# Performance work log

Measured on AMD Instinct MI355X. Metric: run time of the kernel, lower is better.

Reference implementation:

```python
import jax, jax.numpy as jnp
import numpy as np

D_MODEL = 4096
N_Q_HEAD = 32
N_KV_HEAD = 8
HEAD_DIM = D_MODEL // N_Q_HEAD  # 128
N_REP = N_Q_HEAD // N_KV_HEAD   # 4
B, T = 2, 2048


def _rope_tables(seq_len, head_dim, dtype=jnp.float32):
    # theta_i = 10000^(-2*(i-1)/d) for i=1..d/2  (matches torch.pow(10000, -2*(arange(1,d/2+1)-1)/d))
    i = jnp.arange(head_dim // 2, dtype=dtype)
    theta = jnp.power(10000.0, -2.0 * i / head_dim)
    angles = jnp.outer(jnp.arange(seq_len, dtype=dtype), theta)  # [T, d/2]
    return jnp.cos(angles), jnp.sin(angles)


def _apply_rope(x, cos, sin):
    # x: [B, T, h, HD]; pairs are consecutive elements (view_as_complex semantics)
    B_, T_, h, hd = x.shape
    xp = x.reshape(B_, T_, h, hd // 2, 2)
    xr, xi = xp[..., 0], xp[..., 1]
    c = cos[None, :T_, None, :]
    s = sin[None, :T_, None, :]
    out_r = xr * c - xi * s
    out_i = xr * s + xi * c
    return jnp.stack([out_r, out_i], axis=-1).reshape(B_, T_, h, hd)


def setup_inputs() -> dict:
    key = jax.random.key(0)
    ks = jax.random.split(key, 5)
    scale = 0.02
    x = jax.random.normal(ks[0], (B, T, D_MODEL), dtype=jnp.float32)
    wq = jax.random.normal(ks[1], (D_MODEL, N_Q_HEAD * HEAD_DIM), dtype=jnp.float32) * scale
    wk = jax.random.normal(ks[2], (D_MODEL, N_KV_HEAD * HEAD_DIM), dtype=jnp.float32) * scale
    wv = jax.random.normal(ks[3], (D_MODEL, N_KV_HEAD * HEAD_DIM), dtype=jnp.float32) * scale
    wo = jax.random.normal(ks[4], (N_Q_HEAD * HEAD_DIM, D_MODEL), dtype=jnp.float32) * scale
    # causal mask: 1 where masked (strict upper triangle), per masked_fill(mask==1, -inf)
    attention_mask = jnp.triu(jnp.ones((T, T), dtype=jnp.int32), k=1)
    return {"x": x, "wq": wq, "wk": wk, "wv": wv, "wo": wo, "attention_mask": attention_mask}


def reference(x, wq, wk, wv, wo, attention_mask):
    B_, T_, _ = x.shape
    xq = (x @ wq).reshape(B_, T_, N_Q_HEAD, HEAD_DIM)
    xk = (x @ wk).reshape(B_, T_, N_KV_HEAD, HEAD_DIM)
    xv = (x @ wv).reshape(B_, T_, N_KV_HEAD, HEAD_DIM)

    cos, sin = _rope_tables(T_, HEAD_DIM, x.dtype)
    xq = _apply_rope(xq, cos, sin)
    xk = _apply_rope(xk, cos, sin)

    # GQA: repeat kv heads (training path: no cache)
    xk = jnp.repeat(xk, N_REP, axis=2)  # [B, T, HQ, HD]
    xv = jnp.repeat(xv, N_REP, axis=2)

    q = xq.transpose(0, 2, 1, 3)  # [B, H, T, HD]
    k = xk.transpose(0, 2, 1, 3)
    v = xv.transpose(0, 2, 1, 3)

    scores = jnp.einsum('bhqd,bhkd->bhqk', q, k) / jnp.sqrt(jnp.asarray(HEAD_DIM, x.dtype))
    scores = jnp.where(attention_mask[None, None, :, :] == 1, -jnp.inf, scores)
    probs = jax.nn.softmax(scores, axis=-1)
    out = jnp.einsum('bhqk,bhkd->bhqd', probs, v)
    out = out.transpose(0, 2, 1, 3).reshape(B_, T_, N_Q_HEAD * HEAD_DIM)
    return out @ wo
```

## Files before the change

### kernel.cpp

```cpp
#include <hip/hip_runtime.h>
#include <hip/hip_bf16.h>
#include <math.h>

typedef __hip_bfloat16 bf16;
typedef short bf16x8 __attribute__((ext_vector_type(8)));
typedef float f32x4 __attribute__((ext_vector_type(4)));
typedef unsigned int u32;
typedef unsigned short u16;

#define GLD16(g, l)                                                            \
  __builtin_amdgcn_global_load_lds(                                            \
      (const __attribute__((address_space(1))) void*)(g),                      \
      (__attribute__((address_space(3))) void*)(l), 16, 0, 0)

__global__ void convert_f32_bf16(const float* __restrict__ in,
                                 bf16* __restrict__ out) {
  size_t i = ((size_t)blockIdx.x * 256 + threadIdx.x) * 4;
  float4 v = *(const float4*)(in + i);
  out[i + 0] = __float2bfloat16(v.x);
  out[i + 1] = __float2bfloat16(v.y);
  out[i + 2] = __float2bfloat16(v.z);
  out[i + 3] = __float2bfloat16(v.w);
}

__global__ void transpose_f32_bf16(const float* __restrict__ in,
                                   bf16* __restrict__ out, int R, int C) {
  __shared__ bf16 tile[32][33];
  int tx = threadIdx.x & 31, ty = threadIdx.x >> 5;
  int c0 = blockIdx.x * 32, r0 = blockIdx.y * 32;
#pragma unroll
  for (int i = 0; i < 32; i += 8)
    tile[ty + i][tx] = __float2bfloat16(in[(size_t)(r0 + ty + i) * C + c0 + tx]);
  __syncthreads();
#pragma unroll
  for (int i = 0; i < 32; i += 8)
    out[(size_t)(c0 + ty + i) * R + r0 + tx] = tile[tx][ty + i];
}

__global__ void transpose_v(const bf16* __restrict__ V, bf16* __restrict__ VT) {
  __shared__ bf16 tile[32][33];
  int s = blockIdx.z, b = s >> 3, kvh = s & 7;
  int t0 = blockIdx.x * 32, d0 = blockIdx.y * 32;
  int tx = threadIdx.x & 31, ty = threadIdx.x >> 5;
#pragma unroll
  for (int i = 0; i < 32; i += 8)
    tile[ty + i][tx] =
        V[(size_t)(b * 2048 + t0 + ty + i) * 6144 + kvh * 128 + d0 + tx];
  __syncthreads();
#pragma unroll
  for (int i = 0; i < 32; i += 8)
    VT[((size_t)s * 128 + d0 + ty + i) * 2048 + t0 + tx] = tile[tx][ty + i];
}

__global__ void rope_table_k(float* __restrict__ tab) {
  int idx = blockIdx.x * 256 + threadIdx.x;
  int t = idx >> 6, i = idx & 63;
  float theta = powf(10000.0f, -2.0f * (float)i / 128.0f);
  float ang = (float)t * theta;
  tab[idx * 2 + 0] = cosf(ang);
  tab[idx * 2 + 1] = sinf(ang);
}

__global__ void rope_apply(bf16* __restrict__ X, const float* __restrict__ tab,
                           int nheads, int rowstride, float omul) {
  size_t idx = (size_t)blockIdx.x * 256 + threadIdx.x;
  int i = (int)(idx & 63);
  size_t rest = idx >> 6;
  int h = (int)(rest % nheads);
  size_t r = rest / nheads;
  int t = (int)(r & 2047);
  float c = tab[(t * 64 + i) * 2 + 0];
  float s = tab[(t * 64 + i) * 2 + 1];
  bf16* p = X + r * (size_t)rowstride + h * 128 + 2 * i;
  float xr = __bfloat162float(p[0]), xi = __bfloat162float(p[1]);
  p[0] = __float2bfloat16((xr * c - xi * s) * omul);
  p[1] = __float2bfloat16((xr * s + xi * c) * omul);
}

template <typename OutT>
__global__ __launch_bounds__(256, 3) void gemm_bt(const bf16* __restrict__ A,
                                                  const bf16* __restrict__ BT,
                                                  OutT* __restrict__ C, int M,
                                                  int N, int K) {
  __shared__ bf16 As[128 * 32];
  __shared__ bf16 Bs[128 * 32];
  const int tid = threadIdx.x;
  const int lane = tid & 63, w = tid >> 6;
  const int wr = w >> 1, wc = w & 1;
  const int lr = lane & 15;
  const int ko = (lane >> 4) * 8;
  const int m0 = blockIdx.y * 128, n0 = blockIdx.x * 128;

  f32x4 acc[4][4];
#pragma unroll
  for (int m = 0; m < 4; ++m)
#pragma unroll
    for (int n = 0; n < 4; ++n)
#pragma unroll
      for (int j = 0; j < 4; ++j) acc[m][n][j] = 0.f;

  for (int k0 = 0; k0 < K; k0 += 32) {
#pragma unroll
    for (int i = 0; i < 2; ++i) {
      int c = i * 256 + tid;
      const bf16* ga = A + (size_t)(m0 + (c >> 2)) * K + k0 + (c & 3) * 8;
      const bf16* gb = BT + (size_t)(n0 + (c >> 2)) * K + k0 + (c & 3) * 8;
      GLD16(ga, As + c * 8);
      GLD16(gb, Bs + c * 8);
    }
    __syncthreads();
    bf16x8 af[4], bfr[4];
#pragma unroll
    for (int m = 0; m < 4; ++m)
      af[m] = *(const bf16x8*)(As + (wr * 64 + m * 16 + lr) * 32 + ko);
#pragma unroll
    for (int n = 0; n < 4; ++n)
      bfr[n] = *(const bf16x8*)(Bs + (wc * 64 + n * 16 + lr) * 32 + ko);
#pragma unroll
    for (int m = 0; m < 4; ++m)
#pragma unroll
      for (int n = 0; n < 4; ++n)
        acc[m][n] = __builtin_amdgcn_mfma_f32_16x16x32_bf16(af[m], bfr[n],
                                                            acc[m][n], 0, 0, 0);
    __syncthreads();
  }
#pragma unroll
  for (int m = 0; m < 4; ++m) {
    int row_base = m0 + wr * 64 + m * 16 + (lane >> 4) * 4;
#pragma unroll
    for (int n = 0; n < 4; ++n) {
      int col = n0 + wc * 64 + n * 16 + lr;
#pragma unroll
      for (int j = 0; j < 4; ++j) {
        float v = acc[m][n][j];
        if constexpr (sizeof(OutT) == 2)
          C[(size_t)(row_base + j) * N + col] = (OutT)__float2bfloat16(v);
        else
          C[(size_t)(row_base + j) * N + col] = (OutT)v;
      }
    }
  }
}

static __device__ inline u32 cvtpk_bf16(float a, float b) {
  u32 r;
  asm("v_cvt_pk_bf16_f32 %0, %1, %2" : "=v"(r) : "v"(a), "v"(b));
  return r;
}

__global__ __launch_bounds__(256) void flash_attn2(const bf16* __restrict__ Q,
                                                   const bf16* __restrict__ K,
                                                   const bf16* __restrict__ VT,
                                                   bf16* __restrict__ AO) {
  __shared__ bf16 Kbuf[2][64 * 128];
  __shared__ bf16 Vbuf[2][128 * 64];

  int bid = blockIdx.x;
  int lid = (bid & 7) * 128 + (bid >> 3);
  int qt = 15 - (lid & 15);
  int hq = (lid >> 4) & 3;
  int kvh = (lid >> 6) & 7;
  int b = lid >> 9;
  int h = kvh * 4 + hq;

  const int tid = threadIdx.x;
  const int lane = tid & 63, w = tid >> 6;
  const int lr = lane & 15, hi = lane >> 4;
  const int ko = hi * 8;
  const int qrow0 = qt * 128 + w * 32;
  const int nt = 2 * qt + 2;

  const bf16* Kg0 = K + (size_t)b * 2048 * 6144 + kvh * 128;
  const bf16* Vg0 = VT + (size_t)(b * 8 + kvh) * 128 * 2048;

  bf16x8 qf[2][4];
#pragma unroll
  for (int mi = 0; mi < 2; ++mi) {
    const bf16* qb = Q + (size_t)(b * 2048 + qrow0 + mi * 16 + lr) * 6144 + h * 128;
#pragma unroll
    for (int kk = 0; kk < 4; ++kk) qf[mi][kk] = *(const bf16x8*)(qb + kk * 32 + ko);
  }

  f32x4 O[2][8];
  float m_[2], l_[2];
#pragma unroll
  for (int mi = 0; mi < 2; ++mi) {
    m_[mi] = -1e30f;
    l_[mi] = 0.f;
#pragma unroll
    for (int dd = 0; dd < 8; ++dd)
#pragma unroll
      for (int j = 0; j < 4; ++j) O[mi][dd][j] = 0.f;
  }

  auto STAGE = [&](int buf, int kv0) {
    bf16* Ks = &Kbuf[buf][0];
    bf16* Vs = &Vbuf[buf][0];
    const bf16* Kg = Kg0 + (size_t)kv0 * 6144;
    const bf16* Vg = Vg0 + kv0;
#pragma unroll
    for (int it = 0; it < 4; ++it) {
      int s = it * 256 + tid;
      int row = s >> 4, c = s & 15;
      GLD16(Kg + (size_t)row * 6144 + ((c ^ (row & 7)) << 3), Ks + s * 8);
    }
#pragma unroll
    for (int it = 0; it < 4; ++it) {
      int s = it * 256 + tid;
      int row = s >> 3, c = s & 7;
      GLD16(Vg + (size_t)row * 2048 + ((c ^ (row & 7)) << 3), Vs + s * 8);
    }
  };

  STAGE(0, 0);
  __syncthreads();

  for (int t = 0; t < nt; ++t) {
    int kv0 = t * 64;
    if (t + 1 < nt) STAGE((t + 1) & 1, kv0 + 64);

    if (kv0 <= qrow0 + 31) {
      const bf16* Ks = &Kbuf[t & 1][0];
      const bf16* Vs = &Vbuf[t & 1][0];

      f32x4 Sx[2][4];
#pragma unroll
      for (int mi = 0; mi < 2; ++mi)
#pragma unroll
        for (int cb = 0; cb < 4; ++cb)
#pragma unroll
          for (int j = 0; j < 4; ++j) Sx[mi][cb][j] = 0.f;

      __builtin_amdgcn_s_setprio(1);
#pragma unroll
      for (int cb = 0; cb < 4; ++cb) {
        bf16x8 kf[4];
#pragma unroll
        for (int kk = 0; kk < 4; ++kk)
          kf[kk] = *(const bf16x8*)(Ks + (cb * 16 + lr) * 128 +
                                    (((kk * 4 + hi) ^ (lr & 7)) << 3));
#pragma unroll
        for (int mi = 0; mi < 2; ++mi)
#pragma unroll
          for (int kk = 0; kk < 4; ++kk)
            Sx[mi][cb] = __builtin_amdgcn_mfma_f32_16x16x32_bf16(
                kf[kk], qf[mi][kk], Sx[mi][cb], 0, 0, 0);
      }
      __builtin_amdgcn_s_setprio(0);

      bool domask = (kv0 + 63 > qrow0);
      u32 pau[2][2][4];
#pragma unroll
      for (int mi = 0; mi < 2; ++mi) {
        int q = qrow0 + mi * 16 + lr;
        if (domask) {
#pragma unroll
          for (int cb = 0; cb < 4; ++cb)
#pragma unroll
            for (int j = 0; j < 4; ++j)
              if (kv0 + cb * 16 + hi * 4 + j > q) Sx[mi][cb][j] = -1e30f;
        }
        float pm = -1e30f;
#pragma unroll
        for (int cb = 0; cb < 4; ++cb)
#pragma unroll
          for (int j = 0; j < 4; ++j) pm = fmaxf(pm, Sx[mi][cb][j]);
        pm = fmaxf(pm, __shfl_xor(pm, 16));
        pm = fmaxf(pm, __shfl_xor(pm, 32));

        if (!__all(pm - m_[mi] <= 11.5416f)) {
          float nm = fmaxf(m_[mi], pm);
          float rs = exp2f(m_[mi] - nm);
          m_[mi] = nm;
          l_[mi] *= rs;
#pragma unroll
          for (int dd = 0; dd < 8; ++dd)
#pragma unroll
            for (int j = 0; j < 4; ++j) O[mi][dd][j] *= rs;
        }
        float mcur = m_[mi];
        float ps = 0.f;
#pragma unroll
        for (int cb = 0; cb < 4; ++cb)
#pragma unroll
          for (int j = 0; j < 4; ++j) {
            float p = exp2f(Sx[mi][cb][j] - mcur);
            Sx[mi][cb][j] = p;
            ps += p;
          }
        ps += __shfl_xor(ps, 16);
        ps += __shfl_xor(ps, 32);
        l_[mi] += ps;

        u32 vp[8];
#pragma unroll
        for (int cb = 0; cb < 4; ++cb)
#pragma unroll
          for (int jp = 0; jp < 2; ++jp)
            vp[cb * 2 + jp] = cvtpk_bf16(Sx[mi][cb][2 * jp], Sx[mi][cb][2 * jp + 1]);

#pragma unroll
        for (int kk2 = 0; kk2 < 2; ++kk2)
#pragma unroll
          for (int e = 0; e < 4; ++e) {
            int src = lr + ((hi & 1) << 5) + ((e >> 1) << 4);
            u32 va = (u32)__shfl((int)vp[4 * kk2 + (e & 1)], src);
            u32 vb = (u32)__shfl((int)vp[4 * kk2 + 2 + (e & 1)], src);
            pau[mi][kk2][e] = (hi & 2) ? vb : va;
          }
      }

      __builtin_amdgcn_s_setprio(1);
#pragma unroll
      for (int dd = 0; dd < 8; ++dd) {
        bf16x8 vf[2];
#pragma unroll
        for (int kk2 = 0; kk2 < 2; ++kk2)
          vf[kk2] = *(const bf16x8*)(Vs + (dd * 16 + lr) * 64 +
                                     (((kk2 * 4 + hi) ^ (lr & 7)) << 3));
#pragma unroll
        for (int mi = 0; mi < 2; ++mi)
#pragma unroll
          for (int kk2 = 0; kk2 < 2; ++kk2) {
            union { u32 u[4]; bf16x8 h; } cv;
#pragma unroll
            for (int e = 0; e < 4; ++e) cv.u[e] = pau[mi][kk2][e];
            O[mi][dd] = __builtin_amdgcn_mfma_f32_16x16x32_bf16(
                vf[kk2], cv.h, O[mi][dd], 0, 0, 0);
          }
      }
      __builtin_amdgcn_s_setprio(0);
    }
    __syncthreads();
  }

#pragma unroll
  for (int mi = 0; mi < 2; ++mi) {
    float inv = 1.0f / l_[mi];
    bf16* outp = AO + (size_t)(b * 2048 + qrow0 + mi * 16 + lr) * 4096 + h * 128;
#pragma unroll
    for (int dd = 0; dd < 8; ++dd) {
      union { u16 s[4]; unsigned long long v; } pk;
#pragma unroll
      for (int j = 0; j < 4; ++j)
        pk.s[j] = __bfloat16_as_ushort(__float2bfloat16(O[mi][dd][j] * inv));
      *(unsigned long long*)(outp + dd * 16 + hi * 4) = pk.v;
    }
  }
}

extern "C" void kernel_launch(void* const* d_in, const int* in_sizes, int n_in,
                              void* d_out, int out_size, void* d_ws,
                              size_t ws_size, hipStream_t stream) {
  const float* x = (const float*)d_in[0];
  const float* wq = (const float*)d_in[1];
  const float* wk = (const float*)d_in[2];
  const float* wv = (const float*)d_in[3];
  const float* wo = (const float*)d_in[4];

  char* ws = (char*)d_ws;
  bf16* xb    = (bf16*)(ws + 0);
  bf16* WqkvT = (bf16*)(ws + 33554432);
  bf16* WoT   = (bf16*)(ws + 83886080);
  bf16* QKV   = (bf16*)(ws + 117440512);
  bf16* VTb   = (bf16*)(ws + 167772160);
  float* tab  = (float*)(ws + 176160768);
  bf16* AOb   = xb;

  const float LOG2E = 1.4426950408889634f;
  const float ISQ = 0.08838834764831845f;

  convert_f32_bf16<<<16384, 256, 0, stream>>>(x, xb);
  transpose_f32_bf16<<<dim3(128, 128), 256, 0, stream>>>(wq, WqkvT, 4096, 4096);
  transpose_f32_bf16<<<dim3(32, 128), 256, 0, stream>>>(
      wk, WqkvT + (size_t)4096 * 4096, 4096, 1024);
  transpose_f32_bf16<<<dim3(32, 128), 256, 0, stream>>>(
      wv, WqkvT + (size_t)5120 * 4096, 4096, 1024);
  transpose_f32_bf16<<<dim3(128, 128), 256, 0, stream>>>(wo, WoT, 4096, 4096);
  rope_table_k<<<512, 256, 0, stream>>>(tab);

  gemm_bt<bf16><<<dim3(48, 32), 256, 0, stream>>>(xb, WqkvT, QKV, 4096, 6144,
                                                  4096);

  rope_apply<<<32768, 256, 0, stream>>>(QKV, tab, 32, 6144, LOG2E * ISQ);
  rope_apply<<<8192, 256, 0, stream>>>(QKV + 4096, tab, 8, 6144, 1.0f);

  transpose_v<<<dim3(64, 4, 16), 256, 0, stream>>>(QKV + 5120, VTb);

  flash_attn2<<<1024, 256, 0, stream>>>(QKV, QKV + 4096, VTb, AOb);

  gemm_bt<float><<<dim3(32, 32), 256, 0, stream>>>(AOb, WoT, (float*)d_out,
                                                   4096, 4096, 4096);
}
```

Before: 718.2 us.

## Replace GEMM with 256x256 double-buffered 8-wave pipelined kernel

Replaces the simple 128x128, K=32, single-buffered GEMM with a 256x256 tile, K=64, 512-thread kernel. It double-buffers LDS with async global-to-LDS loads interleaved between MFMA phases, uses an XOR-swizzled LDS layout to avoid bank conflicts, raises MFMA priority, and remaps blocks for better L2 locality. The goal is to hide global load latency and raise MFMA utilization in both projection GEMMs. In exchange it uses much more LDS (128KB per block) and more accumulator registers, which lowers occupancy, and it relies on fine-grained manual barriers and vmcnt waits.

Result: faster. 667.1 us (-7.1%).

```diff
diff --git a/kernel.cpp b/kernel.cpp
--- a/kernel.cpp
+++ b/kernel.cpp
@@ -12,6 +12,9 @@
   __builtin_amdgcn_global_load_lds(                                            \
       (const __attribute__((address_space(1))) void*)(g),                      \
       (__attribute__((address_space(3))) void*)(l), 16, 0, 0)
+
+#define BARRIER() asm volatile("s_barrier" ::: "memory")
+#define VMCNT(n) asm volatile("s_waitcnt vmcnt(" #n ")" ::: "memory")
 
 __global__ void convert_f32_bf16(const float* __restrict__ in,
                                  bf16* __restrict__ out) {
@@ -78,58 +81,126 @@
 }
 
 template <typename OutT>
-__global__ __launch_bounds__(256, 3) void gemm_bt(const bf16* __restrict__ A,
-                                                  const bf16* __restrict__ BT,
-                                                  OutT* __restrict__ C, int M,
-                                                  int N, int K) {
-  __shared__ bf16 As[128 * 32];
-  __shared__ bf16 Bs[128 * 32];
+__global__ __launch_bounds__(512, 2) void gemm_bt8(const bf16* __restrict__ A,
+                                                   const bf16* __restrict__ BT,
+                                                   OutT* __restrict__ C, int M,
+                                                   int N, int K) {
+  __shared__ bf16 AS[2][2][128 * 64];
+  __shared__ bf16 BS[2][2][128 * 64];
+
   const int tid = threadIdx.x;
-  const int lane = tid & 63, w = tid >> 6;
-  const int wr = w >> 1, wc = w & 1;
-  const int lr = lane & 15;
-  const int ko = (lane >> 4) * 8;
-  const int m0 = blockIdx.y * 128, n0 = blockIdx.x * 128;
-
-  f32x4 acc[4][4];
-#pragma unroll
-  for (int m = 0; m < 4; ++m)
+  const int lane = tid & 63;
+  const int w = tid >> 6, wm = w >> 2, wn = w & 3;
+  const int lr = lane & 15, hi = lane >> 4;
+
+  int gx = gridDim.x;
+  int nwg = gx * gridDim.y;
+  int bid = blockIdx.y * gx + blockIdx.x;
+  int swz = (bid & 7) * (nwg >> 3) + (bid >> 3);
+  const int m0 = (swz / gx) * 256, n0 = (swz % gx) * 256;
+
+  const int NKT = K >> 6;
+  const int NI = K >> 7;
+  const int srow = tid >> 3;
+  const int scol = ((tid & 7) ^ (srow & 7)) << 3;
+
+  f32x4 acc[8][4];
+#pragma unroll
+  for (int m = 0; m < 8; ++m)
 #pragma unroll
     for (int n = 0; n < 4; ++n)
 #pragma unroll
       for (int j = 0; j < 4; ++j) acc[m][n][j] = 0.f;
 
-  for (int k0 = 0; k0 < K; k0 += 32) {
-#pragma unroll
-    for (int i = 0; i < 2; ++i) {
-      int c = i * 256 + tid;
-      const bf16* ga = A + (size_t)(m0 + (c >> 2)) * K + k0 + (c & 3) * 8;
-      const bf16* gb = BT + (size_t)(n0 + (c >> 2)) * K + k0 + (c & 3) * 8;
-      GLD16(ga, As + c * 8);
-      GLD16(gb, Bs + c * 8);
-    }
-    __syncthreads();
-    bf16x8 af[4], bfr[4];
-#pragma unroll
-    for (int m = 0; m < 4; ++m)
-      af[m] = *(const bf16x8*)(As + (wr * 64 + m * 16 + lr) * 32 + ko);
-#pragma unroll
-    for (int n = 0; n < 4; ++n)
-      bfr[n] = *(const bf16x8*)(Bs + (wc * 64 + n * 16 + lr) * 32 + ko);
-#pragma unroll
-    for (int m = 0; m < 4; ++m)
-#pragma unroll
-      for (int n = 0; n < 4; ++n)
-        acc[m][n] = __builtin_amdgcn_mfma_f32_16x16x32_bf16(af[m], bfr[n],
-                                                            acc[m][n], 0, 0, 0);
-    __syncthreads();
-  }
-#pragma unroll
-  for (int m = 0; m < 4; ++m) {
-    int row_base = m0 + wr * 64 + m * 16 + (lane >> 4) * 4;
+  auto STAGE_A = [&](int buf, int kt) {
+    int kk0 = (kt < NKT) ? kt * 64 : 0;
+#pragma unroll
+    for (int hs = 0; hs < 4; ++hs) {
+      int ha = hs >> 1, sa = hs & 1;
+      const bf16* g = A + (size_t)(m0 + ha * 128 + sa * 64 + srow) * K + kk0 + scol;
+      GLD16(g, &AS[buf][ha][(sa * 64 + srow) * 64 + (tid & 7) * 8]);
+    }
+  };
+  auto STAGE_B = [&](int buf, int kt, int half) {
+    int kk0 = (kt < NKT) ? kt * 64 : 0;
+#pragma unroll
+    for (int sa = 0; sa < 2; ++sa) {
+      const bf16* g =
+          BT + (size_t)(n0 + half * 128 + sa * 64 + srow) * K + kk0 + scol;
+      GLD16(g, &BS[buf][half][(sa * 64 + srow) * 64 + (tid & 7) * 8]);
+    }
+  };
+
+  bf16x8 bfr[4][2], af[2][2];
+  auto READ_B = [&](int buf) {
 #pragma unroll
     for (int n = 0; n < 4; ++n) {
-      int col = n0 + wc * 64 + n * 16 + lr;
+      int row = (wn & 1) * 64 + n * 16 + lr;
+#pragma unroll
+      for (int kk = 0; kk < 2; ++kk)
+        bfr[n][kk] = *(const bf16x8*)(&BS[buf][wn >> 1]
+                                         [row * 64 + (((kk * 4 + hi) ^ (row & 7)) << 3)]);
+    }
+  };
+  auto READ_A = [&](int buf, int q) {
+#pragma unroll
+    for (int mm = 0; mm < 2; ++mm) {
+      int row = (q * 2 + mm) * 16 + lr;
+#pragma unroll
+      for (int kk = 0; kk < 2; ++kk)
+        af[mm][kk] = *(const bf16x8*)(&AS[buf][wm]
+                                         [row * 64 + (((kk * 4 + hi) ^ (row & 7)) << 3)]);
+    }
+  };
+
+#define MFMA16(q)                                                              \
+  do {                                                                         \
+    __builtin_amdgcn_s_setprio(1);                                             \
+    _Pragma("unroll") for (int mm = 0; mm < 2; ++mm)                           \
+        _Pragma("unroll") for (int n = 0; n < 4; ++n)                          \
+        _Pragma("unroll") for (int kk = 0; kk < 2; ++kk)                       \
+            acc[(q) * 2 + mm][n] = __builtin_amdgcn_mfma_f32_16x16x32_bf16(    \
+                af[mm][kk], bfr[n][kk], acc[(q) * 2 + mm][n], 0, 0, 0);        \
+    __builtin_amdgcn_s_setprio(0);                                             \
+  } while (0)
+
+  STAGE_A(0, 0);
+  STAGE_B(0, 0, 0);
+  STAGE_B(0, 0, 1);
+  STAGE_B(1, 1, 0);
+  STAGE_B(1, 1, 1);
+  VMCNT(4);
+  BARRIER();
+
+  for (int i = 0; i < NI; ++i) {
+    int t = 2 * i;
+    READ_B(0); READ_A(0, 0); STAGE_A(1, t + 1);
+    BARRIER(); MFMA16(0); BARRIER();
+    READ_A(0, 1); STAGE_B(0, t + 2, 0);
+    BARRIER(); MFMA16(1); BARRIER();
+    READ_A(0, 2); STAGE_B(0, t + 2, 1);
+    BARRIER(); MFMA16(2); BARRIER();
+    READ_A(0, 3);
+    BARRIER(); MFMA16(3); VMCNT(4); BARRIER();
+    READ_B(1); READ_A(1, 0); STAGE_A(0, t + 2);
+    BARRIER(); MFMA16(0); BARRIER();
+    READ_A(1, 1); STAGE_B(1, t + 3, 0);
+    BARRIER(); MFMA16(1); BARRIER();
+    READ_A(1, 2); STAGE_B(1, t + 3, 1);
+    BARRIER(); MFMA16(2); BARRIER();
+    READ_A(1, 3);
+    BARRIER(); MFMA16(3); VMCNT(4); BARRIER();
+  }
+
+  VMCNT(0);
+  BARRIER();
+
+#pragma unroll
+  for (int m = 0; m < 8; ++m) {
+    int row_base = m0 + wm * 128 + m * 16 + hi * 4;
+#pragma unroll
+    for (int n = 0; n < 4; ++n) {
+      int col = n0 + wn * 64 + n * 16 + lr;
 #pragma unroll
       for (int j = 0; j < 4; ++j) {
         float v = acc[m][n][j];
@@ -140,6 +211,7 @@
       }
     }
   }
+#undef MFMA16
 }
 
 static __device__ inline u32 cvtpk_bf16(float a, float b) {
@@ -379,8 +451,8 @@
   transpose_f32_bf16<<<dim3(128, 128), 256, 0, stream>>>(wo, WoT, 4096, 4096);
   rope_table_k<<<512, 256, 0, stream>>>(tab);
 
-  gemm_bt<bf16><<<dim3(48, 32), 256, 0, stream>>>(xb, WqkvT, QKV, 4096, 6144,
-                                                  4096);
+  gemm_bt8<bf16><<<dim3(24, 16), 512, 0, stream>>>(xb, WqkvT, QKV, 4096, 6144,
+                                                   4096);
 
   rope_apply<<<32768, 256, 0, stream>>>(QKV, tab, 32, 6144, LOG2E * ISQ);
   rope_apply<<<8192, 256, 0, stream>>>(QKV + 4096, tab, 8, 6144, 1.0f);
@@ -389,6 +461,6 @@
 
   flash_attn2<<<1024, 256, 0, stream>>>(QKV, QKV + 4096, VTb, AOb);
 
-  gemm_bt<float><<<dim3(32, 32), 256, 0, stream>>>(AOb, WoT, (float*)d_out,
-                                                   4096, 4096, 4096);
-}
+  gemm_bt8<float><<<dim3(16, 16), 512, 0, stream>>>(AOb, WoT, (float*)d_out,
+                                                    4096, 4096, 4096);
+}
```
